# Kernel tuning notes

Hardware: AMD Instinct MI355X
Metric: run time of the kernel (lower is better)

Reference implementation:

```python
import jax, jax.numpy as jnp
import numpy as np

LN2PI = float(np.log(2.0 * np.pi))
B, T, S = 256, 4096, 32


def setup_inputs() -> dict:
    key = jax.random.key(0)
    ks = jax.random.split(key, 6)
    obvs = jax.random.normal(ks[0], (B, T, 1), jnp.float32)
    ln_pi = jnp.ones((S,), jnp.float32) / S  # CategoricalPrior init: ones/num_states
    trans_w = 1.0 + 0.1 * jax.random.normal(ks[1], (S,), jnp.float32)  # diagonal
    trans_b = 0.1 * jax.random.normal(ks[2], (S,), jnp.float32)
    mu = jax.random.normal(ks[3], (S,), jnp.float32)
    log_sigma = 0.1 * jax.random.normal(ks[4], (S,), jnp.float32)
    return {"obvs": obvs, "ln_pi": ln_pi, "trans_w": trans_w,
            "trans_b": trans_b, "mu": mu, "log_sigma": log_sigma}


def reference(obvs, ln_pi, trans_w, trans_b, mu, log_sigma):
    # GaussianEmbedding: per-state Gaussian log-likelihood -> (B, T, S)
    z = (obvs - mu) * jnp.exp(-log_sigma)
    ln_e = -0.5 * z * z - log_sigma - 0.5 * LN2PI
    ln_e_t = jnp.swapaxes(ln_e, 0, 1)  # (T, B, S), time-major for scan

    # forward recurrence: f_t = emit_t + (w * f_{t-1} + b)
    f0 = ln_e_t[0] + ln_pi
    def fstep(carry, emit):
        nxt = emit + trans_w * carry + trans_b
        return nxt, nxt
    _, fs = jax.lax.scan(fstep, f0, ln_e_t[1:])
    ln_fs = jnp.concatenate([f0[None], fs], axis=0)  # (T, B, S)

    # backward recurrence: b_t = w * (b_{t+1} + emit_{t+1}) + b, b_{T-1} = emit_{T-1} + ln_pi
    bT = ln_e_t[-1] + ln_pi
    def bstep(carry, emit):
        nxt = trans_w * (carry + emit) + trans_b
        return nxt, nxt
    _, bs = jax.lax.scan(bstep, bT, ln_e_t[1:], reverse=True)  # bs[t] = b_t, t in [0, T-2]
    ln_bs = jnp.concatenate([bs, bT[None]], axis=0)  # (T, B, S)

    log_gamma = ln_fs + ln_bs
    log_gamma = log_gamma - jax.nn.logsumexp(log_gamma, axis=2, keepdims=True)
    return jnp.swapaxes(log_gamma, 0, 1)  # (B, T, S)
```

## Files before the change

### kernel.cpp

```cpp
#include <hip/hip_runtime.h>
#include <math.h>

constexpr int Bn = 256;
constexpr int Tn = 4096;
constexpr int Sn = 32;
constexpr int NE = 8;
constexpr int EL = Tn / NE;
constexpr int NT2 = 256;
constexpr int TCN = NT2 / Sn;
constexpr int TL = EL / TCN;
constexpr int CL = 16;
constexpr int CPT = TL / CL;
constexpr float HALF_LN2PI = 0.918938533204672742f;
constexpr float SAT = -3.0e38f;
constexpr float PCLAMP = 1.0e38f;

constexpr size_t OFF_LF = 0;
constexpr size_t OFF_LB = (size_t)Bn * NE * Sn;


#define DPP_ROR_ADD(x, ctrl) \
    ((x) + __int_as_float(__builtin_amdgcn_update_dpp(0, __float_as_int(x), (ctrl), 0xF, 0xF, false)))

__global__ __launch_bounds__(NT2, 8) void hmm_agg_kernel(
    const float* __restrict__ obvs, const float* __restrict__ ln_pi,
    const float* __restrict__ trans_w, const float* __restrict__ trans_b,
    const float* __restrict__ mu, const float* __restrict__ log_sigma,
    float* __restrict__ ws)
{
    __shared__ __align__(16) float s_obvs[EL];
    __shared__ float s_PF[TCN][Sn];
    __shared__ float s_ZB[TCN][Sn];

    const int be  = blockIdx.x;
    const int b   = be >> 3;
    const int e   = be & (NE - 1);
    const int tid = threadIdx.x;
    const int s   = tid & 31;
    const int tc  = tid >> 5;
    const int t0  = tc * TL;

    if (tid < EL / 4)
        ((float4*)s_obvs)[tid] = ((const float4*)(obvs + (size_t)b * Tn + (size_t)e * EL))[tid];

    const float w  = trans_w[s];
    const float tb = trans_b[s];
    const float pi = ln_pi[s];
    const float m  = mu[s];
    const float ls = log_sigma[s];
    const float inv = __expf(-ls);
    const float cqa  = -0.5f * inv * inv;
    const float cqb  = m * inv * inv;
    const float cqcb = -ls - HALF_LN2PI - 0.5f * m * m * inv * inv + tb;
    const float tbb  = tb - w * tb;
    float w16; { float w2 = w * w, w4 = w2 * w2; float w8 = w4 * w4; w16 = w8 * w8; }
    const float w32 = fminf(w16 * w16, PCLAMP);
    const float W64 = fminf(w32 * w32, PCLAMP);
    const bool th0  = (e == 0) && (tc == 0);

    __syncthreads();

#define EMIT(xv) fmaf(fmaf(cqa, (xv), cqb), (xv), cqcb)

    float lbs[CPT];
    float AF = 0.f;
#pragma unroll
    for (int i = 0; i < CPT; ++i) {
        const float4* q4 = (const float4*)(s_obvs + t0 + i * CL);
        float4 v0 = q4[0], v1 = q4[1], v2 = q4[2], v3 = q4[3];
        float x[CL] = {v0.x, v0.y, v0.z, v0.w, v1.x, v1.y, v1.z, v1.w,
                       v2.x, v2.y, v2.z, v2.w, v3.x, v3.y, v3.z, v3.w};
#pragma unroll
        for (int j = 0; j < CL; ++j) {
            float g = EMIT(x[j]);
            if (th0 && i == 0 && j == 0) g += pi - tb;
            AF = fmaf(w, AF, g);
        }
        float l = 0.f;
#pragma unroll
        for (int j = CL - 2; j >= -1; --j)
            l = fmaf(w, l + EMIT(x[j + 1]), tbb);
        lbs[i] = l;
    }
    const float Z3 = lbs[3];
    const float Z2 = fmaf(w16, Z3, lbs[2]);
    const float Z1 = fmaf(w16, Z2, lbs[1]);
    const float ZT = fmaf(w16, Z1, lbs[0]);

    s_PF[tc][s] = AF;
    s_ZB[tc][s] = ZT;
    __syncthreads();

    {
        float Wd = W64;
#pragma unroll
        for (int r = 0; r < 3; ++r) {
            const int d = 1 << r;
            float tF = (tc >= d)      ? s_PF[tc - d][s] : 0.f;
            float tB = (tc + d < TCN) ? s_ZB[tc + d][s] : 0.f;
            __syncthreads();
            if (tc >= d)      s_PF[tc][s] = fmaf(Wd, tF, s_PF[tc][s]);
            if (tc + d < TCN) s_ZB[tc][s] = fmaf(Wd, tB, s_ZB[tc][s]);
            Wd = fminf(Wd * Wd, PCLAMP);
            __syncthreads();
        }
    }

    if (tc == 7) ws[OFF_LF + (size_t)be * Sn + s] = s_PF[TCN - 1][s];
    if (tc == 0) ws[OFF_LB + (size_t)be * Sn + s] = s_ZB[0][s];
#undef EMIT
}

__global__ __launch_bounds__(NT2, 8) void hmm_main_kernel(
    const float* __restrict__ obvs, const float* __restrict__ ln_pi,
    const float* __restrict__ trans_w, const float* __restrict__ trans_b,
    const float* __restrict__ mu, const float* __restrict__ log_sigma,
    float* __restrict__ out, const float* __restrict__ ws)
{
    __shared__ __align__(16) float s_obvs[EL];
    __shared__ float s_PF[TCN][Sn];
    __shared__ float s_ZB[TCN][Sn];

    const int be  = blockIdx.x;
    const int b   = be >> 3;
    const int e   = be & (NE - 1);
    const int tid = threadIdx.x;
    const int s   = tid & 31;
    const int tc  = tid >> 5;
    const int t0  = tc * TL;

    if (tid < EL / 4)
        ((float4*)s_obvs)[tid] = ((const float4*)(obvs + (size_t)b * Tn + (size_t)e * EL))[tid];

    const float w  = trans_w[s];
    const float tb = trans_b[s];
    const float pi = ln_pi[s];
    const float m  = mu[s];
    const float ls = log_sigma[s];
    const float inv = __expf(-ls);
    const float cqa  = -0.5f * inv * inv;
    const float cqb  = m * inv * inv;
    const float cqcb = -ls - HALF_LN2PI - 0.5f * m * m * inv * inv + tb;
    const float tbb  = tb - w * tb;
    float w16; { float w2 = w * w, w4 = w2 * w2; float w8 = w4 * w4; w16 = w8 * w8; }
    const float w32 = fminf(w16 * w16, PCLAMP);
    const float w48 = fminf(w32 * w16, PCLAMP);
    const float W64 = fminf(w32 * w32, PCLAMP);
    const float l2w = log2f(w);
    const float WEL = fminf(exp2f(l2w * 512.0f), PCLAMP);
    const float pY  = fminf(exp2f(l2w * (float)(TL * tc)), PCLAMP);
    const float pX  = fminf(exp2f(l2w * (float)(TL * (7 - tc))), PCLAMP);
    const bool th0  = (e == 0) && (tc == 0);

    __syncthreads();

#define EMIT(xv) fmaf(fmaf(cqa, (xv), cqb), (xv), cqcb)

    float lbs[CPT];
    float AF = 0.f;
#pragma unroll
    for (int i = 0; i < CPT; ++i) {
        const float4* q4 = (const float4*)(s_obvs + t0 + i * CL);
        float4 v0 = q4[0], v1 = q4[1], v2 = q4[2], v3 = q4[3];
        float x[CL] = {v0.x, v0.y, v0.z, v0.w, v1.x, v1.y, v1.z, v1.w,
                       v2.x, v2.y, v2.z, v2.w, v3.x, v3.y, v3.z, v3.w};
#pragma unroll
        for (int j = 0; j < CL; ++j) x[j] = EMIT(x[j]);
#pragma unroll
        for (int j = 0; j < CL; ++j) {
            float g = x[j];
            if (th0 && i == 0 && j == 0) g += pi - tb;
            AF = fmaf(w, AF, g);
        }
        float l = 0.f;
#pragma unroll
        for (int j = CL - 2; j >= -1; --j)
            l = fmaf(w, l + x[j + 1], tbb);
        lbs[i] = l;
    }
    const float Z3 = lbs[3];
    const float Z2 = fmaf(w16, Z3, lbs[2]);
    const float Z1 = fmaf(w16, Z2, lbs[1]);
    const float ZT = fmaf(w16, Z1, lbs[0]);

    s_PF[tc][s] = AF;
    s_ZB[tc][s] = ZT;
    __syncthreads();

    {
        float Wd = W64;
#pragma unroll
        for (int r = 0; r < 3; ++r) {
            const int d = 1 << r;
            float tF = (tc >= d)      ? s_PF[tc - d][s] : 0.f;
            float tB = (tc + d < TCN) ? s_ZB[tc + d][s] : 0.f;
            __syncthreads();
            if (tc >= d)      s_PF[tc][s] = fmaf(Wd, tF, s_PF[tc][s]);
            if (tc + d < TCN) s_ZB[tc][s] = fmaf(Wd, tB, s_ZB[tc][s]);
            Wd = fminf(Wd * Wd, PCLAMP);
            __syncthreads();
        }
    }

    float Y = 0.f;
#pragma unroll
    for (int qq = 0; qq < NE - 1; ++qq)
        if (qq < e) Y = fmaf(WEL, Y, ws[OFF_LF + (size_t)(b * NE + qq) * Sn + s]);
    float xT = obvs[(size_t)b * Tn + Tn - 1];
    float X = EMIT(xT) + (pi - tb);
#pragma unroll
    for (int qq = NE - 1; qq > 0; --qq)
        if (qq > e) X = fmaf(WEL, X, ws[OFF_LB + (size_t)(b * NE + qq) * Sn + s]);

    const float Pprev  = (tc > 0)       ? s_PF[tc - 1][s] : 0.f;
    const float ZSnext = (tc < TCN - 1) ? s_ZB[tc + 1][s] : 0.f;
    float f         = fmaf(pY, Y, Pprev);
    const float Xth = fmaf(pX, X, ZSnext);
    float Rarr[CPT];
    Rarr[3] = Xth;
    Rarr[2] = fmaf(w16, Xth, Z3);
    Rarr[1] = fmaf(w32, Xth, Z2);
    Rarr[0] = fmaf(w48, Xth, Z1);

    const size_t rowbase = (size_t)b * Tn + (size_t)e * EL;
    float* outp = out + ((rowbase + t0) << 5) + s;

#pragma unroll
    for (int i = 0; i < CPT; ++i) {
        const float4* q4 = (const float4*)(s_obvs + t0 + i * CL);
        float4 v0 = q4[0], v1 = q4[1], v2 = q4[2], v3 = q4[3];
        float x[CL] = {v0.x, v0.y, v0.z, v0.w, v1.x, v1.y, v1.z, v1.w,
                       v2.x, v2.y, v2.z, v2.w, v3.x, v3.y, v3.z, v3.w};
#pragma unroll
        for (int j = 0; j < CL; ++j) x[j] = EMIT(x[j]);
        if (th0 && i == 0) x[0] += pi - tb;

        float barr[CL];
        barr[CL - 1] = Rarr[i];
#pragma unroll
        for (int j = CL - 2; j >= 0; --j)
            barr[j] = fmaf(w, barr[j + 1] + x[j + 1], tbb);

#pragma unroll
        for (int j = 0; j < CL; ++j) {
            f = fmaf(w, f, x[j]);
            float v = f + barr[j];
            float sum = __expf(v);
            sum = DPP_ROR_ADD(sum, 0x121);
            sum = DPP_ROR_ADD(sum, 0x122);
            sum = DPP_ROR_ADD(sum, 0x124);
            sum = DPP_ROR_ADD(sum, 0x128);
            sum += __shfl_xor(sum, 16, 32);
            sum = fmaxf(sum, 1.0e-35f);
            outp[(size_t)(i * CL + j) << 5] = fmaxf(v - __logf(sum), SAT);
        }
    }
#undef EMIT
}

extern "C" void kernel_launch(void* const* d_in, const int* in_sizes, int n_in,
                              void* d_out, int out_size, void* d_ws, size_t ws_size,
                              hipStream_t stream)
{
    const float* obvs      = (const float*)d_in[0];
    const float* ln_pi     = (const float*)d_in[1];
    const float* trans_w   = (const float*)d_in[2];
    const float* trans_b   = (const float*)d_in[3];
    const float* mu        = (const float*)d_in[4];
    const float* log_sigma = (const float*)d_in[5];
    float* out = (float*)d_out;
    float* wsf = (float*)d_ws;

    hipLaunchKernelGGL(hmm_agg_kernel, dim3(Bn * NE), dim3(NT2), 0, stream,
                       obvs, ln_pi, trans_w, trans_b, mu, log_sigma, wsf);
    hipLaunchKernelGGL(hmm_main_kernel, dim3(Bn * NE), dim3(NT2), 0, stream,
                       obvs, ln_pi, trans_w, trans_b, mu, log_sigma, out, wsf);
}
```

Before: 47.38 us.

## Map two states per thread with 16 time groups in HMM main kernel

Each thread in the main kernel now owns two adjacent states instead of one, and the block splits its time segment into 16 groups of 32 steps instead of 8 groups of 64. The per-timestep logsumexp over the 32 states then fits within a 16-lane DPP row (quad_perm, half-mirror, row rotate), which drops the cross-row shuffle. It also issues one log per two outputs and writes float2 stores. In exchange there is more register pressure from the duplicated state recurrences, a fourth scan round in shared memory, and the launch-bounds occupancy hint has been removed.

```diff
diff --git a/kernel.cpp b/kernel.cpp
--- a/kernel.cpp
+++ b/kernel.cpp
@@ -7,10 +7,14 @@
 constexpr int NE = 8;
 constexpr int EL = Tn / NE;
 constexpr int NT2 = 256;
-constexpr int TCN = NT2 / Sn;
-constexpr int TL = EL / TCN;
+constexpr int TCN = 8;
+constexpr int TL = 64;
 constexpr int CL = 16;
-constexpr int CPT = TL / CL;
+constexpr int CPT = 4;
+constexpr int NG  = 16;
+constexpr int GW  = EL / NG;
+constexpr int CL2 = 8;
+constexpr int CPT2 = GW / CL2;
 constexpr float HALF_LN2PI = 0.918938533204672742f;
 constexpr float SAT = -3.0e38f;
 constexpr float PCLAMP = 1.0e38f;
@@ -19,7 +23,7 @@
 constexpr size_t OFF_LB = (size_t)Bn * NE * Sn;
 
 
-#define DPP_ROR_ADD(x, ctrl) \
+#define DPP_ADD(x, ctrl) \
     ((x) + __int_as_float(__builtin_amdgcn_update_dpp(0, __float_as_int(x), (ctrl), 0xF, 0xF, false)))
 
 __global__ __launch_bounds__(NT2, 8) void hmm_agg_kernel(
@@ -111,151 +115,185 @@
 #undef EMIT
 }
 
-__global__ __launch_bounds__(NT2, 8) void hmm_main_kernel(
+__global__ __launch_bounds__(NT2) void hmm_main_kernel(
     const float* __restrict__ obvs, const float* __restrict__ ln_pi,
     const float* __restrict__ trans_w, const float* __restrict__ trans_b,
     const float* __restrict__ mu, const float* __restrict__ log_sigma,
     float* __restrict__ out, const float* __restrict__ ws)
 {
     __shared__ __align__(16) float s_obvs[EL];
-    __shared__ float s_PF[TCN][Sn];
-    __shared__ float s_ZB[TCN][Sn];
+    __shared__ __align__(8) float s_PF[NG][Sn];
+    __shared__ __align__(8) float s_ZB[NG][Sn];
 
     const int be  = blockIdx.x;
     const int b   = be >> 3;
     const int e   = be & (NE - 1);
     const int tid = threadIdx.x;
-    const int s   = tid & 31;
-    const int tc  = tid >> 5;
-    const int t0  = tc * TL;
+    const int sp  = tid & 15;
+    const int g   = tid >> 4;
+    const int s0  = 2 * sp;
+    const int t0  = g * GW;
 
     if (tid < EL / 4)
         ((float4*)s_obvs)[tid] = ((const float4*)(obvs + (size_t)b * Tn + (size_t)e * EL))[tid];
 
-    const float w  = trans_w[s];
-    const float tb = trans_b[s];
-    const float pi = ln_pi[s];
-    const float m  = mu[s];
-    const float ls = log_sigma[s];
-    const float inv = __expf(-ls);
-    const float cqa  = -0.5f * inv * inv;
-    const float cqb  = m * inv * inv;
-    const float cqcb = -ls - HALF_LN2PI - 0.5f * m * m * inv * inv + tb;
-    const float tbb  = tb - w * tb;
-    float w16; { float w2 = w * w, w4 = w2 * w2; float w8 = w4 * w4; w16 = w8 * w8; }
-    const float w32 = fminf(w16 * w16, PCLAMP);
-    const float w48 = fminf(w32 * w16, PCLAMP);
-    const float W64 = fminf(w32 * w32, PCLAMP);
-    const float l2w = log2f(w);
-    const float WEL = fminf(exp2f(l2w * 512.0f), PCLAMP);
-    const float pY  = fminf(exp2f(l2w * (float)(TL * tc)), PCLAMP);
-    const float pX  = fminf(exp2f(l2w * (float)(TL * (7 - tc))), PCLAMP);
-    const bool th0  = (e == 0) && (tc == 0);
+    const float2 wv  = *(const float2*)&trans_w[s0];
+    const float2 tbv = *(const float2*)&trans_b[s0];
+    const float2 piv = *(const float2*)&ln_pi[s0];
+    const float2 muv = *(const float2*)&mu[s0];
+    const float2 lsv = *(const float2*)&log_sigma[s0];
+    const float inv0 = __expf(-lsv.x), inv1 = __expf(-lsv.y);
+    const float cqa0 = -0.5f * inv0 * inv0,          cqa1 = -0.5f * inv1 * inv1;
+    const float cqb0 = muv.x * inv0 * inv0,          cqb1 = muv.y * inv1 * inv1;
+    const float cqc0 = -lsv.x - HALF_LN2PI - 0.5f * muv.x * muv.x * inv0 * inv0 + tbv.x;
+    const float cqc1 = -lsv.y - HALF_LN2PI - 0.5f * muv.y * muv.y * inv1 * inv1 + tbv.y;
+    const float tbb0 = tbv.x - wv.x * tbv.x,         tbb1 = tbv.y - wv.y * tbv.y;
+    float w8_0, w8_1;
+    { float a2 = wv.x * wv.x, a4 = a2 * a2; w8_0 = a4 * a4;
+      float b2 = wv.y * wv.y, b4 = b2 * b2; w8_1 = b4 * b4; }
+    const float w16_0 = fminf(w8_0 * w8_0, PCLAMP), w16_1 = fminf(w8_1 * w8_1, PCLAMP);
+    const float w24_0 = fminf(w16_0 * w8_0, PCLAMP), w24_1 = fminf(w16_1 * w8_1, PCLAMP);
+    const float W32_0 = fminf(w16_0 * w16_0, PCLAMP), W32_1 = fminf(w16_1 * w16_1, PCLAMP);
+    const float l2w0 = log2f(wv.x), l2w1 = log2f(wv.y);
+    const float WEL0 = fminf(exp2f(l2w0 * 512.0f), PCLAMP);
+    const float WEL1 = fminf(exp2f(l2w1 * 512.0f), PCLAMP);
+    const float pY0 = fminf(exp2f(l2w0 * (float)(GW * g)), PCLAMP);
+    const float pY1 = fminf(exp2f(l2w1 * (float)(GW * g)), PCLAMP);
+    const float pX0 = fminf(exp2f(l2w0 * (float)(GW * (NG - 1 - g))), PCLAMP);
+    const float pX1 = fminf(exp2f(l2w1 * (float)(GW * (NG - 1 - g))), PCLAMP);
+    const bool th0 = (e == 0) && (g == 0);
 
     __syncthreads();
 
-#define EMIT(xv) fmaf(fmaf(cqa, (xv), cqb), (xv), cqcb)
-
-    float lbs[CPT];
-    float AF = 0.f;
-#pragma unroll
-    for (int i = 0; i < CPT; ++i) {
-        const float4* q4 = (const float4*)(s_obvs + t0 + i * CL);
-        float4 v0 = q4[0], v1 = q4[1], v2 = q4[2], v3 = q4[3];
-        float x[CL] = {v0.x, v0.y, v0.z, v0.w, v1.x, v1.y, v1.z, v1.w,
-                       v2.x, v2.y, v2.z, v2.w, v3.x, v3.y, v3.z, v3.w};
-#pragma unroll
-        for (int j = 0; j < CL; ++j) x[j] = EMIT(x[j]);
-#pragma unroll
-        for (int j = 0; j < CL; ++j) {
-            float g = x[j];
-            if (th0 && i == 0 && j == 0) g += pi - tb;
-            AF = fmaf(w, AF, g);
-        }
-        float l = 0.f;
-#pragma unroll
-        for (int j = CL - 2; j >= -1; --j)
-            l = fmaf(w, l + x[j + 1], tbb);
-        lbs[i] = l;
-    }
-    const float Z3 = lbs[3];
-    const float Z2 = fmaf(w16, Z3, lbs[2]);
-    const float Z1 = fmaf(w16, Z2, lbs[1]);
-    const float ZT = fmaf(w16, Z1, lbs[0]);
-
-    s_PF[tc][s] = AF;
-    s_ZB[tc][s] = ZT;
+#define EMIT0(xv) fmaf(fmaf(cqa0, (xv), cqb0), (xv), cqc0)
+#define EMIT1(xv) fmaf(fmaf(cqa1, (xv), cqb1), (xv), cqc1)
+
+    float lbs0[CPT2], lbs1[CPT2];
+    float AF0 = 0.f, AF1 = 0.f;
+#pragma unroll
+    for (int i = 0; i < CPT2; ++i) {
+        const float4* q4 = (const float4*)(s_obvs + t0 + i * CL2);
+        float4 va = q4[0], vb = q4[1];
+        float x[CL2] = {va.x, va.y, va.z, va.w, vb.x, vb.y, vb.z, vb.w};
+        float e0[CL2];
+#pragma unroll
+        for (int j = 0; j < CL2; ++j) { e0[j] = EMIT0(x[j]); x[j] = EMIT1(x[j]); }
+        if (th0 && i == 0) { e0[0] += piv.x - tbv.x; x[0] += piv.y - tbv.y; }
+#pragma unroll
+        for (int j = 0; j < CL2; ++j) {
+            AF0 = fmaf(wv.x, AF0, e0[j]);
+            AF1 = fmaf(wv.y, AF1, x[j]);
+        }
+        float l0 = 0.f, l1 = 0.f;
+#pragma unroll
+        for (int j = CL2 - 2; j >= -1; --j) {
+            l0 = fmaf(wv.x, l0 + e0[j + 1], tbb0);
+            l1 = fmaf(wv.y, l1 + x[j + 1], tbb1);
+        }
+        lbs0[i] = l0; lbs1[i] = l1;
+    }
+    const float Z3_0 = lbs0[3], Z3_1 = lbs1[3];
+    const float Z2_0 = fmaf(w8_0, Z3_0, lbs0[2]), Z2_1 = fmaf(w8_1, Z3_1, lbs1[2]);
+    const float Z1_0 = fmaf(w8_0, Z2_0, lbs0[1]), Z1_1 = fmaf(w8_1, Z2_1, lbs1[1]);
+    const float ZT0  = fmaf(w8_0, Z1_0, lbs0[0]), ZT1  = fmaf(w8_1, Z1_1, lbs1[0]);
+
+    *(float2*)&s_PF[g][s0] = make_float2(AF0, AF1);
+    *(float2*)&s_ZB[g][s0] = make_float2(ZT0, ZT1);
     __syncthreads();
 
     {
-        float Wd = W64;
-#pragma unroll
-        for (int r = 0; r < 3; ++r) {
+        float Wd0 = W32_0, Wd1 = W32_1;
+#pragma unroll
+        for (int r = 0; r < 4; ++r) {
             const int d = 1 << r;
-            float tF = (tc >= d)      ? s_PF[tc - d][s] : 0.f;
-            float tB = (tc + d < TCN) ? s_ZB[tc + d][s] : 0.f;
+            float2 tF = (g >= d)     ? *(const float2*)&s_PF[g - d][s0] : make_float2(0.f, 0.f);
+            float2 tB = (g + d < NG) ? *(const float2*)&s_ZB[g + d][s0] : make_float2(0.f, 0.f);
             __syncthreads();
-            if (tc >= d)      s_PF[tc][s] = fmaf(Wd, tF, s_PF[tc][s]);
-            if (tc + d < TCN) s_ZB[tc][s] = fmaf(Wd, tB, s_ZB[tc][s]);
-            Wd = fminf(Wd * Wd, PCLAMP);
+            if (g >= d) {
+                s_PF[g][s0]     = fmaf(Wd0, tF.x, s_PF[g][s0]);
+                s_PF[g][s0 + 1] = fmaf(Wd1, tF.y, s_PF[g][s0 + 1]);
+            }
+            if (g + d < NG) {
+                s_ZB[g][s0]     = fmaf(Wd0, tB.x, s_ZB[g][s0]);
+                s_ZB[g][s0 + 1] = fmaf(Wd1, tB.y, s_ZB[g][s0 + 1]);
+            }
+            Wd0 = fminf(Wd0 * Wd0, PCLAMP);
+            Wd1 = fminf(Wd1 * Wd1, PCLAMP);
             __syncthreads();
         }
     }
 
-    float Y = 0.f;
+    float Y0 = 0.f, Y1 = 0.f;
 #pragma unroll
     for (int qq = 0; qq < NE - 1; ++qq)
-        if (qq < e) Y = fmaf(WEL, Y, ws[OFF_LF + (size_t)(b * NE + qq) * Sn + s]);
+        if (qq < e) {
+            float2 L = *(const float2*)&ws[OFF_LF + (size_t)(b * NE + qq) * Sn + s0];
+            Y0 = fmaf(WEL0, Y0, L.x);
+            Y1 = fmaf(WEL1, Y1, L.y);
+        }
     float xT = obvs[(size_t)b * Tn + Tn - 1];
-    float X = EMIT(xT) + (pi - tb);
+    float X0 = EMIT0(xT) + (piv.x - tbv.x);
+    float X1 = EMIT1(xT) + (piv.y - tbv.y);
 #pragma unroll
     for (int qq = NE - 1; qq > 0; --qq)
-        if (qq > e) X = fmaf(WEL, X, ws[OFF_LB + (size_t)(b * NE + qq) * Sn + s]);
-
-    const float Pprev  = (tc > 0)       ? s_PF[tc - 1][s] : 0.f;
-    const float ZSnext = (tc < TCN - 1) ? s_ZB[tc + 1][s] : 0.f;
-    float f         = fmaf(pY, Y, Pprev);
-    const float Xth = fmaf(pX, X, ZSnext);
-    float Rarr[CPT];
-    Rarr[3] = Xth;
-    Rarr[2] = fmaf(w16, Xth, Z3);
-    Rarr[1] = fmaf(w32, Xth, Z2);
-    Rarr[0] = fmaf(w48, Xth, Z1);
+        if (qq > e) {
+            float2 L = *(const float2*)&ws[OFF_LB + (size_t)(b * NE + qq) * Sn + s0];
+            X0 = fmaf(WEL0, X0, L.x);
+            X1 = fmaf(WEL1, X1, L.y);
+        }
+
+    float2 Pp = (g > 0)      ? *(const float2*)&s_PF[g - 1][s0] : make_float2(0.f, 0.f);
+    float2 Zn = (g < NG - 1) ? *(const float2*)&s_ZB[g + 1][s0] : make_float2(0.f, 0.f);
+    float f0 = fmaf(pY0, Y0, Pp.x);
+    float f1 = fmaf(pY1, Y1, Pp.y);
+    const float Xth0 = fmaf(pX0, X0, Zn.x);
+    const float Xth1 = fmaf(pX1, X1, Zn.y);
+    float R0[CPT2], R1[CPT2];
+    R0[3] = Xth0;                 R1[3] = Xth1;
+    R0[2] = fmaf(w8_0,  Xth0, Z3_0); R1[2] = fmaf(w8_1,  Xth1, Z3_1);
+    R0[1] = fmaf(w16_0, Xth0, Z2_0); R1[1] = fmaf(w16_1, Xth1, Z2_1);
+    R0[0] = fmaf(w24_0, Xth0, Z1_0); R1[0] = fmaf(w24_1, Xth1, Z1_1);
 
     const size_t rowbase = (size_t)b * Tn + (size_t)e * EL;
-    float* outp = out + ((rowbase + t0) << 5) + s;
-
-#pragma unroll
-    for (int i = 0; i < CPT; ++i) {
-        const float4* q4 = (const float4*)(s_obvs + t0 + i * CL);
-        float4 v0 = q4[0], v1 = q4[1], v2 = q4[2], v3 = q4[3];
-        float x[CL] = {v0.x, v0.y, v0.z, v0.w, v1.x, v1.y, v1.z, v1.w,
-                       v2.x, v2.y, v2.z, v2.w, v3.x, v3.y, v3.z, v3.w};
-#pragma unroll
-        for (int j = 0; j < CL; ++j) x[j] = EMIT(x[j]);
-        if (th0 && i == 0) x[0] += pi - tb;
-
-        float barr[CL];
-        barr[CL - 1] = Rarr[i];
-#pragma unroll
-        for (int j = CL - 2; j >= 0; --j)
-            barr[j] = fmaf(w, barr[j + 1] + x[j + 1], tbb);
-
-#pragma unroll
-        for (int j = 0; j < CL; ++j) {
-            f = fmaf(w, f, x[j]);
-            float v = f + barr[j];
-            float sum = __expf(v);
-            sum = DPP_ROR_ADD(sum, 0x121);
-            sum = DPP_ROR_ADD(sum, 0x122);
-            sum = DPP_ROR_ADD(sum, 0x124);
-            sum = DPP_ROR_ADD(sum, 0x128);
-            sum += __shfl_xor(sum, 16, 32);
+    float* outp = out + ((rowbase + t0) << 5) + s0;
+
+#pragma unroll
+    for (int i = 0; i < CPT2; ++i) {
+        const float4* q4 = (const float4*)(s_obvs + t0 + i * CL2);
+        float4 va = q4[0], vb = q4[1];
+        float x[CL2] = {va.x, va.y, va.z, va.w, vb.x, vb.y, vb.z, vb.w};
+        float e0[CL2];
+#pragma unroll
+        for (int j = 0; j < CL2; ++j) { e0[j] = EMIT0(x[j]); x[j] = EMIT1(x[j]); }
+        if (th0 && i == 0) { e0[0] += piv.x - tbv.x; x[0] += piv.y - tbv.y; }
+
+        float b0[CL2], b1[CL2];
+        b0[CL2 - 1] = R0[i]; b1[CL2 - 1] = R1[i];
+#pragma unroll
+        for (int j = CL2 - 2; j >= 0; --j) {
+            b0[j] = fmaf(wv.x, b0[j + 1] + e0[j + 1], tbb0);
+            b1[j] = fmaf(wv.y, b1[j + 1] + x[j + 1], tbb1);
+        }
+
+#pragma unroll
+        for (int j = 0; j < CL2; ++j) {
+            f0 = fmaf(wv.x, f0, e0[j]);
+            f1 = fmaf(wv.y, f1, x[j]);
+            float v0 = f0 + b0[j];
+            float v1 = f1 + b1[j];
+            float sum = __expf(v0) + __expf(v1);
+            sum = DPP_ADD(sum, 0xB1);
+            sum = DPP_ADD(sum, 0x4E);
+            sum = DPP_ADD(sum, 0x141);
+            sum = DPP_ADD(sum, 0x128);
             sum = fmaxf(sum, 1.0e-35f);
-            outp[(size_t)(i * CL + j) << 5] = fmaxf(v - __logf(sum), SAT);
-        }
-    }
-#undef EMIT
+            float lse = __logf(sum);
+            float2 r = make_float2(fmaxf(v0 - lse, SAT), fmaxf(v1 - lse, SAT));
+            *(float2*)(outp + ((size_t)(i * CL2 + j) << 5)) = r;
+        }
+    }
+#undef EMIT0
+#undef EMIT1
 }
 
 extern "C" void kernel_launch(void* const* d_in, const int* in_sizes, int n_in,
```

Result: faster. 43.61 us (-7.9%).
